# Kernel optimization log

Hardware: AMD Instinct MI355X
Metric: run time of the kernel (lower is better)

The kernel has to match this reference:

```python
import jax, jax.numpy as jnp
import numpy as np

B, S, D, H = 2, 2048, 1024, 16
DEPTH = D // H


def setup_inputs() -> dict:
    key = jax.random.key(0)
    ks = jax.random.split(key, 12)
    scale = 1.0 / np.sqrt(D)
    inp = {
        "v": jax.random.normal(ks[0], (B, S, D), jnp.float32),
        "k": jax.random.normal(ks[1], (B, S, D), jnp.float32),
        "q": jax.random.normal(ks[2], (B, S, D), jnp.float32),
        "mask": jnp.tril(jnp.ones((S, S), jnp.int32))[None, None],  # causal [1,1,S,S]
        "wq_w": jax.random.normal(ks[3], (D, D), jnp.float32) * scale,
        "wq_b": jnp.zeros((D,), jnp.float32),
        "wk_w": jax.random.normal(ks[4], (D, D), jnp.float32) * scale,
        "wk_b": jnp.zeros((D,), jnp.float32),
        "wv_w": jax.random.normal(ks[5], (D, D), jnp.float32) * scale,
        "wv_b": jnp.zeros((D,), jnp.float32),
        "dense_w": jax.random.normal(ks[6], (D, D), jnp.float32) * scale,
        "dense_b": jnp.zeros((D,), jnp.float32),
    }
    return inp


def _split_heads(x):
    # [B, S, D] -> [B, H, S, depth]
    b, s, _ = x.shape
    return x.reshape(b, s, H, DEPTH).transpose(0, 2, 1, 3)


def reference(v, k, q, mask, wq_w, wq_b, wk_w, wk_b, wv_w, wv_b, dense_w, dense_b):
    qh = _split_heads(q @ wq_w.T + wq_b)
    kh = _split_heads(k @ wk_w.T + wk_b)
    vh = _split_heads(v @ wv_w.T + wv_b)
    scores = jnp.einsum("bhqd,bhkd->bhqk", qh, kh) / jnp.sqrt(jnp.float32(DEPTH))
    scores = jnp.where(mask == 0, jnp.float32(-1e9), scores)
    attn = jax.nn.softmax(scores, axis=-1)
    out = jnp.einsum("bhqk,bhkd->bhqd", attn, vh)
    out = out.transpose(0, 2, 1, 3).reshape(q.shape[0], -1, D)
    out = out @ dense_w.T + dense_b
    return (out, attn)
```

## Files before the change

kernel.cpp:

```cpp
#include <hip/hip_runtime.h>
#include <hip/hip_bf16.h>
#include <stdint.h>

#define S_LEN 2048
#define D_DIM 1024
#define NH    16
#define DEPTH 64
#define NB    2

typedef __attribute__((ext_vector_type(8))) short bf16x8;
typedef __attribute__((ext_vector_type(4))) float f32x4;

static __device__ __forceinline__ unsigned short f2b(float f) {
  union { float f; uint32_t u; } v; v.f = f;
  uint32_t u = v.u;
  uint32_t r = (u + 0x7FFFu + ((u >> 16) & 1u)) >> 16;
  return (unsigned short)r;
}

static __device__ __forceinline__ void gload_lds16(const void* g, void* l) {
  __builtin_amdgcn_global_load_lds(
      (const __attribute__((address_space(1))) uint32_t*)g,
      (__attribute__((address_space(3))) uint32_t*)l, 16, 0, 0);
}

#define SWZ(off, row) ((off) ^ (((row) & 7u) << 4))

struct CvtArgs {
  const float* src[7];
  unsigned short* dst[7];
  int n[7];
};

__global__ __launch_bounds__(256) void cvt_kernel(CvtArgs a) {
  const int z = blockIdx.y;
  const float* __restrict__ s = a.src[z];
  unsigned short* __restrict__ d = a.dst[z];
  const int n8 = a.n[z] >> 3;
  const int stride = gridDim.x * 256;
  for (int i = blockIdx.x * 256 + threadIdx.x; i < n8; i += stride) {
    const float4* sp = (const float4*)(s + (size_t)i * 8);
    float4 x = sp[0], y = sp[1];
    union { unsigned short u[8]; uint4 v; } o;
    o.u[0] = f2b(x.x); o.u[1] = f2b(x.y); o.u[2] = f2b(x.z); o.u[3] = f2b(x.w);
    o.u[4] = f2b(y.x); o.u[5] = f2b(y.y); o.u[6] = f2b(y.z); o.u[7] = f2b(y.w);
    *(uint4*)(d + (size_t)i * 8) = o.v;
  }
}

struct GemmArgs {
  const unsigned short* A[3];
  const unsigned short* Bw[3];
  const float* bias[3];
  void* C[3];
  int M, N, K;
  int out_f32;
};

__global__ __launch_bounds__(256) void gemm_bt_kernel(GemmArgs g) {
  const int z = blockIdx.z;
  const unsigned short* __restrict__ A = g.A[z];
  const unsigned short* __restrict__ Bw = g.Bw[z];
  const float* __restrict__ bias = g.bias[z];
  const int K = g.K, N = g.N;
  const int tid = threadIdx.x, lane = tid & 63, wave = tid >> 6;
  const int wr = wave >> 1, wc = wave & 1;
  const int l15 = lane & 15, l4 = lane >> 4;
  const int brow = blockIdx.y * 128, bcol = blockIdx.x * 128;

  __shared__ unsigned short lsA[128 * 64];
  __shared__ unsigned short lsB[128 * 64];

  f32x4 acc[4][4];
#pragma unroll
  for (int i = 0; i < 4; ++i)
#pragma unroll
    for (int j = 0; j < 4; ++j) acc[i][j] = (f32x4){0.f, 0.f, 0.f, 0.f};

  for (int kt = 0; kt < K; kt += 64) {
    __syncthreads();
#pragma unroll
    for (int i = 0; i < 4; ++i) {
      int c = tid + i * 256;
      int row = c >> 3;
      int lb = (int)(SWZ((uint32_t)(c * 16), (uint32_t)row) & 127u);
      gload_lds16(A + (size_t)(brow + row) * K + kt + (lb >> 1),
                  (char*)lsA + (size_t)c * 16);
      gload_lds16(Bw + (size_t)(bcol + row) * K + kt + (lb >> 1),
                  (char*)lsB + (size_t)c * 16);
    }
    __syncthreads();
#pragma unroll
    for (int kc = 0; kc < 2; ++kc) {
      bf16x8 af[4], bfr[4];
#pragma unroll
      for (int mf = 0; mf < 4; ++mf) {
        uint32_t r = (uint32_t)(wr * 64 + mf * 16 + l15);
        uint32_t off = r * 128 + (uint32_t)(kc * 64 + l4 * 16);
        af[mf] = *(const bf16x8*)((const char*)lsA + SWZ(off, r));
      }
#pragma unroll
      for (int nf = 0; nf < 4; ++nf) {
        uint32_t r = (uint32_t)(wc * 64 + nf * 16 + l15);
        uint32_t off = r * 128 + (uint32_t)(kc * 64 + l4 * 16);
        bfr[nf] = *(const bf16x8*)((const char*)lsB + SWZ(off, r));
      }
#pragma unroll
      for (int mf = 0; mf < 4; ++mf)
#pragma unroll
        for (int nf = 0; nf < 4; ++nf)
          acc[mf][nf] = __builtin_amdgcn_mfma_f32_16x16x32_bf16(
              af[mf], bfr[nf], acc[mf][nf], 0, 0, 0);
    }
  }

  const int of32 = g.out_f32;
#pragma unroll
  for (int nf = 0; nf < 4; ++nf) {
    int gcol = bcol + wc * 64 + nf * 16 + l15;
    float bv = bias[gcol];
#pragma unroll
    for (int mf = 0; mf < 4; ++mf) {
#pragma unroll
      for (int r = 0; r < 4; ++r) {
        int grow = brow + wr * 64 + mf * 16 + l4 * 4 + r;
        float vv = acc[mf][nf][r] + bv;
        if (of32)
          ((float*)g.C[z])[(size_t)grow * N + gcol] = vv;
        else
          ((unsigned short*)g.C[z])[(size_t)grow * N + gcol] = f2b(vv);
      }
    }
  }
}

__global__ __launch_bounds__(256) void flash_kernel(
    const unsigned short* __restrict__ Qp, const unsigned short* __restrict__ Kp,
    const unsigned short* __restrict__ Vp, float* __restrict__ stats,
    unsigned short* __restrict__ ctx) {
  const int bh = blockIdx.x;
  const int b = bh >> 4, h = bh & 15;
  const int rt = (int)gridDim.y - 1 - (int)blockIdx.y;
  const int tid = threadIdx.x, lane = tid & 63, w = tid >> 6;
  const int l15 = lane & 15, l4 = lane >> 4;
  const int myrow0 = w * 16 + l4 * 4;

  __shared__ unsigned short lsQ[64 * 64];
  __shared__ unsigned short lsK[64 * 64];
  __shared__ unsigned short lsV[64 * 64];
  __shared__ unsigned short lsP[64 * 64];

  const size_t base = (size_t)b * S_LEN * D_DIM + (size_t)h * DEPTH;

#pragma unroll
  for (int i = 0; i < 2; ++i) {
    int c = tid + i * 256;
    int row = c >> 3;
    int lb = (int)(SWZ((uint32_t)(c * 16), (uint32_t)row) & 127u);
    gload_lds16(Qp + base + (size_t)(rt * 64 + row) * D_DIM + (lb >> 1),
                (char*)lsQ + (size_t)c * 16);
  }
  __syncthreads();
  bf16x8 qf[2];
#pragma unroll
  for (int kc = 0; kc < 2; ++kc) {
    uint32_t r = (uint32_t)(w * 16 + l15);
    uint32_t off = r * 128 + (uint32_t)(kc * 64 + l4 * 16);
    qf[kc] = *(const bf16x8*)((const char*)lsQ + SWZ(off, r));
  }

  float l_run[4] = {0.f, 0.f, 0.f, 0.f};
  f32x4 oacc[4];
#pragma unroll
  for (int df = 0; df < 4; ++df) oacc[df] = (f32x4){0.f, 0.f, 0.f, 0.f};

  for (int ct = 0; ct <= rt; ++ct) {
    __syncthreads();
#pragma unroll
    for (int i = 0; i < 2; ++i) {
      int c = tid + i * 256;
      int row = c >> 3;
      int lb = (int)(SWZ((uint32_t)(c * 16), (uint32_t)row) & 127u);
      gload_lds16(Kp + base + (size_t)(ct * 64 + row) * D_DIM + (lb >> 1),
                  (char*)lsK + (size_t)c * 16);
    }
    {
      const unsigned short* vs = Vp + base + (size_t)(ct * 64 + lane) * D_DIM + w * 16;
      bf16x8 v0 = *(const bf16x8*)vs;
      bf16x8 v1 = *(const bf16x8*)(vs + 8);
#pragma unroll
      for (int j = 0; j < 8; ++j) {
        uint32_t d0 = (uint32_t)(w * 16 + j);
        *(unsigned short*)((char*)lsV + SWZ(d0 * 128 + lane * 2, d0)) =
            (unsigned short)v0[j];
        uint32_t d1 = (uint32_t)(w * 16 + 8 + j);
        *(unsigned short*)((char*)lsV + SWZ(d1 * 128 + lane * 2, d1)) =
            (unsigned short)v1[j];
      }
    }
    __syncthreads();
    f32x4 sacc[4];
#pragma unroll
    for (int nf = 0; nf < 4; ++nf) sacc[nf] = (f32x4){0.f, 0.f, 0.f, 0.f};
#pragma unroll
    for (int kc = 0; kc < 2; ++kc) {
#pragma unroll
      for (int nf = 0; nf < 4; ++nf) {
        uint32_t r = (uint32_t)(nf * 16 + l15);
        uint32_t off = r * 128 + (uint32_t)(kc * 64 + l4 * 16);
        bf16x8 kf = *(const bf16x8*)((const char*)lsK + SWZ(off, r));
        sacc[nf] = __builtin_amdgcn_mfma_f32_16x16x32_bf16(qf[kc], kf, sacc[nf], 0, 0, 0);
      }
    }
    const bool diag = (ct == rt);
    float st[4] = {0.f, 0.f, 0.f, 0.f};
#pragma unroll
    for (int nf = 0; nf < 4; ++nf) {
      int gcol = ct * 64 + nf * 16 + l15;
#pragma unroll
      for (int r = 0; r < 4; ++r) {
        int lrow = myrow0 + r;
        float p = (diag && gcol > rt * 64 + lrow)
                      ? 0.f
                      : __expf(sacc[nf][r] * 0.125f);
        st[r] += p;
        uint32_t off = (uint32_t)lrow * 128 + (uint32_t)(nf * 16 + l15) * 2;
        *(unsigned short*)((char*)lsP + SWZ(off, (uint32_t)lrow)) = f2b(p);
      }
    }
#pragma unroll
    for (int r = 0; r < 4; ++r) {
#pragma unroll
      for (int o = 1; o < 16; o <<= 1) st[r] += __shfl_xor(st[r], o);
      l_run[r] += st[r];
    }
#pragma unroll
    for (int kc = 0; kc < 2; ++kc) {
      uint32_t pr = (uint32_t)(w * 16 + l15);
      uint32_t poff = pr * 128 + (uint32_t)(kc * 64 + l4 * 16);
      bf16x8 pa = *(const bf16x8*)((const char*)lsP + SWZ(poff, pr));
#pragma unroll
      for (int df = 0; df < 4; ++df) {
        uint32_t vr = (uint32_t)(df * 16 + l15);
        uint32_t voff = vr * 128 + (uint32_t)(kc * 64 + l4 * 16);
        bf16x8 vb = *(const bf16x8*)((const char*)lsV + SWZ(voff, vr));
        oacc[df] = __builtin_amdgcn_mfma_f32_16x16x32_bf16(pa, vb, oacc[df], 0, 0, 0);
      }
    }
  }

  float invl[4];
#pragma unroll
  for (int r = 0; r < 4; ++r) invl[r] = 1.f / l_run[r];

  if (l15 == 0) {
#pragma unroll
    for (int r = 0; r < 4; ++r)
      stats[(size_t)bh * S_LEN + rt * 64 + myrow0 + r] = invl[r];
  }

#pragma unroll
  for (int df = 0; df < 4; ++df) {
#pragma unroll
    for (int r = 0; r < 4; ++r) {
      int lrow = myrow0 + r;
      int gd = df * 16 + l15;
      ctx[((size_t)b * S_LEN + rt * 64 + lrow) * D_DIM + h * DEPTH + gd] =
          f2b(oacc[df][r] * invl[r]);
    }
  }
}

__global__ __launch_bounds__(256) void attn_write_kernel(
    const unsigned short* __restrict__ Qp, const unsigned short* __restrict__ Kp,
    const float* __restrict__ stats, float* __restrict__ attn_out) {
  const int ct = blockIdx.x, rt = blockIdx.y, bh = blockIdx.z;
  const int tid = threadIdx.x;
  float* attn_tb = attn_out + ((size_t)bh * S_LEN + (size_t)rt * 64) * S_LEN +
                   (size_t)ct * 64;

  if (ct > rt) {
    float4 z4 = {0.f, 0.f, 0.f, 0.f};
#pragma unroll
    for (int i = 0; i < 4; ++i) {
      int f = tid + i * 256;
      int row = f >> 4, cq = f & 15;
      *(float4*)(attn_tb + (size_t)row * S_LEN + cq * 4) = z4;
    }
    return;
  }

  const int b = bh >> 4, h = bh & 15;
  const int lane = tid & 63, w = tid >> 6;
  const int l15 = lane & 15, l4 = lane >> 4;
  const int myrow0 = w * 16 + l4 * 4;

  __shared__ unsigned short lsQ[64 * 64];
  __shared__ unsigned short lsK[64 * 64];

  const size_t base = (size_t)b * S_LEN * D_DIM + (size_t)h * DEPTH;
#pragma unroll
  for (int i = 0; i < 2; ++i) {
    int c = tid + i * 256;
    int row = c >> 3;
    int lb = (int)(SWZ((uint32_t)(c * 16), (uint32_t)row) & 127u);
    gload_lds16(Qp + base + (size_t)(rt * 64 + row) * D_DIM + (lb >> 1),
                (char*)lsQ + (size_t)c * 16);
    gload_lds16(Kp + base + (size_t)(ct * 64 + row) * D_DIM + (lb >> 1),
                (char*)lsK + (size_t)c * 16);
  }
  __syncthreads();

  bf16x8 qf[2];
#pragma unroll
  for (int kc = 0; kc < 2; ++kc) {
    uint32_t r = (uint32_t)(w * 16 + l15);
    uint32_t off = r * 128 + (uint32_t)(kc * 64 + l4 * 16);
    qf[kc] = *(const bf16x8*)((const char*)lsQ + SWZ(off, r));
  }
  f32x4 sacc[4];
#pragma unroll
  for (int nf = 0; nf < 4; ++nf) sacc[nf] = (f32x4){0.f, 0.f, 0.f, 0.f};
#pragma unroll
  for (int kc = 0; kc < 2; ++kc) {
#pragma unroll
    for (int nf = 0; nf < 4; ++nf) {
      uint32_t r = (uint32_t)(nf * 16 + l15);
      uint32_t off = r * 128 + (uint32_t)(kc * 64 + l4 * 16);
      bf16x8 kf = *(const bf16x8*)((const char*)lsK + SWZ(off, r));
      sacc[nf] = __builtin_amdgcn_mfma_f32_16x16x32_bf16(qf[kc], kf, sacc[nf], 0, 0, 0);
    }
  }

  const float4 invl4 =
      *(const float4*)&stats[(size_t)bh * S_LEN + rt * 64 + myrow0];
  const bool diag = (ct == rt);
#pragma unroll
  for (int nf = 0; nf < 4; ++nf) {
    int gcol = ct * 64 + nf * 16 + l15;
#pragma unroll
    for (int r = 0; r < 4; ++r) {
      int lrow = myrow0 + r;
      float p = (diag && gcol > rt * 64 + lrow)
                    ? 0.f
                    : __expf(sacc[nf][r] * 0.125f) * ((const float*)&invl4)[r];
      attn_tb[(size_t)lrow * S_LEN + (size_t)(nf * 16 + l15)] = p;
    }
  }
}

extern "C" void kernel_launch(void* const* d_in, const int* in_sizes, int n_in,
                              void* d_out, int out_size, void* d_ws, size_t ws_size,
                              hipStream_t stream) {
  const float* v_in = (const float*)d_in[0];
  const float* k_in = (const float*)d_in[1];
  const float* q_in = (const float*)d_in[2];
  const float* wq_w = (const float*)d_in[4];
  const float* wq_b = (const float*)d_in[5];
  const float* wk_w = (const float*)d_in[6];
  const float* wk_b = (const float*)d_in[7];
  const float* wv_w = (const float*)d_in[8];
  const float* wv_b = (const float*)d_in[9];
  const float* wd_w = (const float*)d_in[10];
  const float* wd_b = (const float*)d_in[11];

  char* ws = (char*)d_ws;
  const size_t MB = 1024 * 1024;
  unsigned short* q_bf = (unsigned short*)(ws + 0 * MB);
  unsigned short* k_bf = (unsigned short*)(ws + 8 * MB);
  unsigned short* v_bf = (unsigned short*)(ws + 16 * MB);
  unsigned short* wq_bf = (unsigned short*)(ws + 24 * MB);
  unsigned short* wk_bf = (unsigned short*)(ws + 26 * MB);
  unsigned short* wv_bf = (unsigned short*)(ws + 28 * MB);
  unsigned short* wd_bf = (unsigned short*)(ws + 30 * MB);
  unsigned short* Qp = (unsigned short*)(ws + 32 * MB);
  unsigned short* Kp = (unsigned short*)(ws + 40 * MB);
  unsigned short* Vp = (unsigned short*)(ws + 48 * MB);
  float* stats = (float*)(ws + 56 * MB);
  unsigned short* ctx = (unsigned short*)(ws + 0 * MB);

  float* out = (float*)d_out;
  float* attn = out + (size_t)NB * S_LEN * D_DIM;

  const int n_qkv = NB * S_LEN * D_DIM;
  const int n_w = D_DIM * D_DIM;

  CvtArgs ca;
  ca.src[0] = q_in;  ca.dst[0] = q_bf;  ca.n[0] = n_qkv;
  ca.src[1] = k_in;  ca.dst[1] = k_bf;  ca.n[1] = n_qkv;
  ca.src[2] = v_in;  ca.dst[2] = v_bf;  ca.n[2] = n_qkv;
  ca.src[3] = wq_w;  ca.dst[3] = wq_bf; ca.n[3] = n_w;
  ca.src[4] = wk_w;  ca.dst[4] = wk_bf; ca.n[4] = n_w;
  ca.src[5] = wv_w;  ca.dst[5] = wv_bf; ca.n[5] = n_w;
  ca.src[6] = wd_w;  ca.dst[6] = wd_bf; ca.n[6] = n_w;
  cvt_kernel<<<dim3(1024, 7), dim3(256), 0, stream>>>(ca);

  GemmArgs gq;
  gq.A[0] = q_bf; gq.Bw[0] = wq_bf; gq.bias[0] = wq_b; gq.C[0] = Qp;
  gq.A[1] = k_bf; gq.Bw[1] = wk_bf; gq.bias[1] = wk_b; gq.C[1] = Kp;
  gq.A[2] = v_bf; gq.Bw[2] = wv_bf; gq.bias[2] = wv_b; gq.C[2] = Vp;
  gq.M = NB * S_LEN; gq.N = D_DIM; gq.K = D_DIM; gq.out_f32 = 0;
  gemm_bt_kernel<<<dim3(D_DIM / 128, NB * S_LEN / 128, 3), dim3(256), 0, stream>>>(gq);

  flash_kernel<<<dim3(NB * NH, S_LEN / 64), dim3(256), 0, stream>>>(
      Qp, Kp, Vp, stats, ctx);

  attn_write_kernel<<<dim3(S_LEN / 64, S_LEN / 64, NB * NH), dim3(256), 0,
                      stream>>>(Qp, Kp, stats, attn);

  GemmArgs gd;
  gd.A[0] = ctx; gd.Bw[0] = wd_bf; gd.bias[0] = wd_b; gd.C[0] = out;
  gd.A[1] = nullptr; gd.Bw[1] = nullptr; gd.bias[1] = nullptr; gd.C[1] = nullptr;
  gd.A[2] = nullptr; gd.Bw[2] = nullptr; gd.bias[2] = nullptr; gd.C[2] = nullptr;
  gd.M = NB * S_LEN; gd.N = D_DIM; gd.K = D_DIM; gd.out_f32 = 1;
  gemm_bt_kernel<<<dim3(D_DIM / 128, NB * S_LEN / 128, 1), dim3(256), 0, stream>>>(gd);
}
```

Measured before the change: 755.3 us.

## Pre-transpose V for async LDS loads and stage attn tiles for coalesced writes

Adds a kernel that transposes V per head into a [bh, depth, seq] buffer, so the flash kernel can load V tiles with direct global-to-LDS copies instead of scalar transposing stores into shared memory. The attn write kernel now stages probabilities in a padded shared tile and writes whole float4 rows, replacing scattered per-lane scalar stores to the large attention output. The cost is an extra kernel launch, an extra pass over V, and more shared memory in the attn kernel.

```diff
diff --git a/kernel.cpp b/kernel.cpp
--- a/kernel.cpp
+++ b/kernel.cpp
@@ -134,9 +134,37 @@
   }
 }
 
+__global__ __launch_bounds__(256) void vt_kernel(
+    const unsigned short* __restrict__ Vp, unsigned short* __restrict__ Vt) {
+  const int sc = blockIdx.x, bh = blockIdx.y;
+  const int b = bh >> 4, h = bh & 15;
+  const int tid = threadIdx.x;
+  __shared__ unsigned short t[64][65];
+
+#pragma unroll
+  for (int i = 0; i < 2; ++i) {
+    int row = (tid >> 3) + i * 32;
+    int ch = tid & 7;
+    bf16x8 v = *(const bf16x8*)(Vp + ((size_t)(b * S_LEN + sc * 64 + row)) * D_DIM +
+                                h * DEPTH + ch * 8);
+#pragma unroll
+    for (int j = 0; j < 8; ++j) t[row][ch * 8 + j] = (unsigned short)v[j];
+  }
+  __syncthreads();
+#pragma unroll
+  for (int i = 0; i < 2; ++i) {
+    int d = (tid >> 3) + i * 32;
+    int ch = tid & 7;
+    union { unsigned short u[8]; uint4 v; } o;
+#pragma unroll
+    for (int j = 0; j < 8; ++j) o.u[j] = t[ch * 8 + j][d];
+    *(uint4*)(Vt + ((size_t)bh * DEPTH + d) * S_LEN + sc * 64 + ch * 8) = o.v;
+  }
+}
+
 __global__ __launch_bounds__(256) void flash_kernel(
     const unsigned short* __restrict__ Qp, const unsigned short* __restrict__ Kp,
-    const unsigned short* __restrict__ Vp, float* __restrict__ stats,
+    const unsigned short* __restrict__ Vt, float* __restrict__ stats,
     unsigned short* __restrict__ ctx) {
   const int bh = blockIdx.x;
   const int b = bh >> 4, h = bh & 15;
@@ -151,6 +179,7 @@
   __shared__ unsigned short lsP[64 * 64];
 
   const size_t base = (size_t)b * S_LEN * D_DIM + (size_t)h * DEPTH;
+  const size_t vbase = (size_t)bh * DEPTH * S_LEN;
 
 #pragma unroll
   for (int i = 0; i < 2; ++i) {
@@ -183,20 +212,8 @@
       int lb = (int)(SWZ((uint32_t)(c * 16), (uint32_t)row) & 127u);
       gload_lds16(Kp + base + (size_t)(ct * 64 + row) * D_DIM + (lb >> 1),
                   (char*)lsK + (size_t)c * 16);
-    }
-    {
-      const unsigned short* vs = Vp + base + (size_t)(ct * 64 + lane) * D_DIM + w * 16;
-      bf16x8 v0 = *(const bf16x8*)vs;
-      bf16x8 v1 = *(const bf16x8*)(vs + 8);
-#pragma unroll
-      for (int j = 0; j < 8; ++j) {
-        uint32_t d0 = (uint32_t)(w * 16 + j);
-        *(unsigned short*)((char*)lsV + SWZ(d0 * 128 + lane * 2, d0)) =
-            (unsigned short)v0[j];
-        uint32_t d1 = (uint32_t)(w * 16 + 8 + j);
-        *(unsigned short*)((char*)lsV + SWZ(d1 * 128 + lane * 2, d1)) =
-            (unsigned short)v1[j];
-      }
+      gload_lds16(Vt + vbase + (size_t)row * S_LEN + ct * 64 + (lb >> 1),
+                  (char*)lsV + (size_t)c * 16);
     }
     __syncthreads();
     f32x4 sacc[4];
@@ -297,6 +314,7 @@
 
   __shared__ unsigned short lsQ[64 * 64];
   __shared__ unsigned short lsK[64 * 64];
+  __shared__ float lsT[64][68];
 
   const size_t base = (size_t)b * S_LEN * D_DIM + (size_t)h * DEPTH;
 #pragma unroll
@@ -337,15 +355,22 @@
   const bool diag = (ct == rt);
 #pragma unroll
   for (int nf = 0; nf < 4; ++nf) {
-    int gcol = ct * 64 + nf * 16 + l15;
+    int col = nf * 16 + l15;
 #pragma unroll
     for (int r = 0; r < 4; ++r) {
       int lrow = myrow0 + r;
-      float p = (diag && gcol > rt * 64 + lrow)
+      float p = (diag && col > lrow)
                     ? 0.f
                     : __expf(sacc[nf][r] * 0.125f) * ((const float*)&invl4)[r];
-      attn_tb[(size_t)lrow * S_LEN + (size_t)(nf * 16 + l15)] = p;
-    }
+      lsT[lrow][col] = p;
+    }
+  }
+  __syncthreads();
+#pragma unroll
+  for (int i = 0; i < 4; ++i) {
+    int idx = tid + i * 256;
+    int row = idx >> 4, c4 = idx & 15;
+    *(float4*)(attn_tb + (size_t)row * S_LEN + c4 * 4) = *(float4*)&lsT[row][c4 * 4];
   }
 }
 
@@ -377,6 +402,7 @@
   unsigned short* Kp = (unsigned short*)(ws + 40 * MB);
   unsigned short* Vp = (unsigned short*)(ws + 48 * MB);
   float* stats = (float*)(ws + 56 * MB);
+  unsigned short* Vt = (unsigned short*)(ws + 58 * MB);
   unsigned short* ctx = (unsigned short*)(ws + 0 * MB);
 
   float* out = (float*)d_out;
@@ -402,8 +428,10 @@
   gq.M = NB * S_LEN; gq.N = D_DIM; gq.K = D_DIM; gq.out_f32 = 0;
   gemm_bt_kernel<<<dim3(D_DIM / 128, NB * S_LEN / 128, 3), dim3(256), 0, stream>>>(gq);
 
+  vt_kernel<<<dim3(S_LEN / 64, NB * NH), dim3(256), 0, stream>>>(Vp, Vt);
+
   flash_kernel<<<dim3(NB * NH, S_LEN / 64), dim3(256), 0, stream>>>(
-      Qp, Kp, Vp, stats, ctx);
+      Qp, Kp, Vt, stats, ctx);
 
   attn_write_kernel<<<dim3(S_LEN / 64, S_LEN / 64, NB * NH), dim3(256), 0,
                       stream>>>(Qp, Kp, stats, attn);
```

Result: no change. 761.7 us (+0.8%).
